# Kernel optimization log

Hardware: AMD Instinct MI355X
Metric: run time of the kernel (lower is better)

## Reference

```python
import jax, jax.numpy as jnp
import numpy as np

D = 1024   # model dim
H = 16     # heads
HD = D // H
L = 14     # layers
FF = 4096  # ffn hidden
T = 768    # sequence length


def layer_norm(x, g, b, eps):
    m = x.mean(-1, keepdims=True)
    v = ((x - m) ** 2).mean(-1, keepdims=True)
    return (x - m) / jnp.sqrt(v + eps) * g + b


def rel_pos_emb(t, d):
    # EspnetRelPositionalEncoding: concat(flip(pe_positive), pe_negative[1:]) -> (1, 2t-1, d)
    pos = jnp.arange(t, dtype=jnp.float32)
    div = jnp.exp(jnp.arange(0, d, 2, dtype=jnp.float32) * (-jnp.log(10000.0) / d))
    ang = pos[:, None] * div[None, :]                              # (t, d/2)
    pe_pos = jnp.stack([jnp.sin(ang), jnp.cos(ang)], -1).reshape(t, d)
    pe_neg = jnp.stack([jnp.sin(-ang), jnp.cos(-ang)], -1).reshape(t, d)
    return jnp.concatenate([pe_pos[::-1], pe_neg[1:]], 0)[None]    # (1, 2t-1, d)


def rel_shift(x):
    # x: (b, h, t, 2t-1) -> (b, h, t, t), Transformer-XL shift
    b, h, t, n = x.shape
    xp = jnp.concatenate([jnp.zeros((b, h, t, 1), x.dtype), x], -1)  # (b,h,t,n+1)
    xp = xp.reshape(b, h, n + 1, t)
    x = xp[:, :, 1:].reshape(b, h, t, n)
    return x[..., : n // 2 + 1]


def setup_inputs() -> dict:
    key = jax.random.key(0)
    ks = iter(jax.random.split(key, 40))
    s = 0.02
    nrm = lambda k, shape: jax.random.normal(k, shape, dtype=jnp.float32) * s
    return {
        "xs": jax.random.normal(next(ks), (1, T, D), dtype=jnp.float32),
        "embed_W": nrm(next(ks), (D, D)), "embed_b": jnp.zeros((D,), jnp.float32),
        "embed_ln_g": jnp.ones((D,), jnp.float32), "embed_ln_b": jnp.zeros((D,), jnp.float32),
        "Wq": nrm(next(ks), (L, D, D)), "bq": jnp.zeros((L, D), jnp.float32),
        "Wk": nrm(next(ks), (L, D, D)), "bk": jnp.zeros((L, D), jnp.float32),
        "Wv": nrm(next(ks), (L, D, D)), "bv": jnp.zeros((L, D), jnp.float32),
        "Wo": nrm(next(ks), (L, D, D)), "bo": jnp.zeros((L, D), jnp.float32),
        "Wp": nrm(next(ks), (L, D, D)),
        "pos_u": nrm(next(ks), (L, H, HD)), "pos_v": nrm(next(ks), (L, H, HD)),
        "ln1_g": jnp.ones((L, D), jnp.float32), "ln1_b": jnp.zeros((L, D), jnp.float32),
        "ln2_g": jnp.ones((L, D), jnp.float32), "ln2_b": jnp.zeros((L, D), jnp.float32),
        "ff_W1": nrm(next(ks), (L, D, FF)), "ff_b1": jnp.zeros((L, FF), jnp.float32),
        "ff_W2": nrm(next(ks), (L, FF, D)), "ff_b2": jnp.zeros((L, D), jnp.float32),
        "after_g": jnp.ones((D,), jnp.float32), "after_b": jnp.zeros((D,), jnp.float32),
    }


def reference(xs, embed_W, embed_b, embed_ln_g, embed_ln_b,
              Wq, bq, Wk, bk, Wv, bv, Wo, bo, Wp, pos_u, pos_v,
              ln1_g, ln1_b, ln2_g, ln2_b, ff_W1, ff_b1, ff_W2, ff_b2,
              after_g, after_b):
    b, t, _ = xs.shape
    # LegacyLinearNoSubsampling: Linear -> LayerNorm(eps=1e-5) -> (dropout) -> ReLU
    h = jnp.maximum(layer_norm(xs @ embed_W + embed_b, embed_ln_g, embed_ln_b, 1e-5), 0.0)
    x = h * jnp.sqrt(jnp.float32(D))          # pos-enc scale factor
    pos = rel_pos_emb(t, D)                    # (1, 2t-1, D)
    scale = jnp.float32(HD) ** -0.5
    for i in range(L):
        res = x
        xn = layer_norm(x, ln1_g[i], ln1_b[i], 1e-12)
        q = (xn @ Wq[i] + bq[i]).reshape(b, t, H, HD).transpose(0, 2, 1, 3)   # bhtd
        k = (xn @ Wk[i] + bk[i]).reshape(b, t, H, HD).transpose(0, 2, 1, 3)
        v = (xn @ Wv[i] + bv[i]).reshape(b, t, H, HD).transpose(0, 2, 1, 3)
        p = (pos @ Wp[i]).reshape(1, 2 * t - 1, H, HD).transpose(0, 2, 1, 3)  # bhnd
        ac = jnp.einsum('bhtd,bhsd->bhts', q + pos_u[i][None, :, None, :], k)
        bd = rel_shift(jnp.einsum('bhtd,bhnd->bhtn', q + pos_v[i][None, :, None, :], p))
        attn = jax.nn.softmax((ac + bd) * scale, axis=-1)
        o = jnp.einsum('bhts,bhsd->bhtd', attn, v).transpose(0, 2, 1, 3).reshape(b, t, D)
        x = res + (o @ Wo[i] + bo[i])
        res = x
        xn = layer_norm(x, ln2_g[i], ln2_b[i], 1e-12)
        x = res + (jnp.maximum(xn @ ff_W1[i] + ff_b1[i], 0.0) @ ff_W2[i] + ff_b2[i])
    return layer_norm(x, after_g, after_b, 1e-5)
```

## Files before the change

kernel.cpp:

```cpp
#include <hip/hip_runtime.h>
#include <hip/hip_bf16.h>
#include <math.h>

#define D_    1024
#define H_    16
#define HD_   64
#define L_    14
#define FF_   4096
#define T_    768
#define NPOS_ (2*T_-1)

using s16x8 = __attribute__((ext_vector_type(8))) short;
using f32x4 = __attribute__((ext_vector_type(4))) float;

__device__ inline short f2bf(float f) {
  __hip_bfloat16 h = __float2bfloat16(f);
  return *reinterpret_cast<short*>(&h);
}
__device__ inline float bf2f(unsigned short u) {
  union { unsigned u; float f; } v; v.u = ((unsigned)u) << 16; return v.f;
}

__device__ inline float waveRedSum(float v) {
#pragma unroll
  for (int o = 32; o > 0; o >>= 1) v += __shfl_down(v, o, 64);
  return v;
}
__device__ inline float blockRedSum(float v, float* sh) {
  int lane = threadIdx.x & 63, wid = threadIdx.x >> 6;
  v = waveRedSum(v);
  if (lane == 0) sh[wid] = v;
  __syncthreads();
  if (wid == 0) {
    float x = (lane < 4) ? sh[lane] : 0.f;
    x = waveRedSum(x);
    if (lane == 0) sh[0] = x;
  }
  __syncthreads();
  float r = sh[0];
  __syncthreads();
  return r;
}

__global__ __launch_bounds__(256) void ln_kernel(
    const float* __restrict__ x, const float* __restrict__ g,
    const float* __restrict__ b, void* __restrict__ y,
    float eps, int relu, float scale, int obf)
{
  __shared__ float sh[8];
  long row = blockIdx.x;
  const float* xr = x + row * D_;
  int tid = threadIdx.x;
  float4 v = *(const float4*)&xr[tid * 4];
  float s  = v.x + v.y + v.z + v.w;
  float sq = v.x * v.x + v.y * v.y + v.z * v.z + v.w * v.w;
  float mean = blockRedSum(s, sh) * (1.f / D_);
  float esq  = blockRedSum(sq, sh) * (1.f / D_);
  float var  = esq - mean * mean;
  if (var < 0.f) var = 0.f;
  float inv = rsqrtf(var + eps);
  float4 gv = *(const float4*)&g[tid * 4];
  float4 bv = *(const float4*)&b[tid * 4];
  float o0 = (v.x - mean) * inv * gv.x + bv.x;
  float o1 = (v.y - mean) * inv * gv.y + bv.y;
  float o2 = (v.z - mean) * inv * gv.z + bv.z;
  float o3 = (v.w - mean) * inv * gv.w + bv.w;
  if (relu) {
    o0 = fmaxf(o0, 0.f); o1 = fmaxf(o1, 0.f);
    o2 = fmaxf(o2, 0.f); o3 = fmaxf(o3, 0.f);
  }
  o0 *= scale; o1 *= scale; o2 *= scale; o3 *= scale;
  if (obf) {
    short4 sv;
    sv.x = f2bf(o0); sv.y = f2bf(o1); sv.z = f2bf(o2); sv.w = f2bf(o3);
    *(short4*)&((unsigned short*)y)[row * D_ + tid * 4] = sv;
  } else {
    float4 ov; ov.x = o0; ov.y = o1; ov.z = o2; ov.w = o3;
    *(float4*)&((float*)y)[row * D_ + tid * 4] = ov;
  }
}

__global__ __launch_bounds__(256) void transpose_kernel(
    const float* __restrict__ in, unsigned short* __restrict__ out, int K, int N)
{
  __shared__ unsigned short t[32][33];
  long z = blockIdx.z;
  in  += z * (long)K * N;
  out += z * (long)K * N;
  int n0 = blockIdx.x * 32, k0 = blockIdx.y * 32;
  int tid = threadIdx.x;
  int r = tid >> 3, c4 = (tid & 7) * 4;
  float4 v = *(const float4*)&in[(long)(k0 + r) * N + n0 + c4];
  t[r][c4 + 0] = (unsigned short)f2bf(v.x);
  t[r][c4 + 1] = (unsigned short)f2bf(v.y);
  t[r][c4 + 2] = (unsigned short)f2bf(v.z);
  t[r][c4 + 3] = (unsigned short)f2bf(v.w);
  __syncthreads();
  ushort4 s;
  s.x = t[c4 + 0][r]; s.y = t[c4 + 1][r]; s.z = t[c4 + 2][r]; s.w = t[c4 + 3][r];
  *(ushort4*)&out[(long)(n0 + r) * K + k0 + c4] = s;
}

__global__ __launch_bounds__(256) void transpose5_kernel(
    const float* __restrict__ W0, const float* __restrict__ W1,
    const float* __restrict__ W2, const float* __restrict__ W3,
    const float* __restrict__ W4,
    unsigned short* __restrict__ O0, unsigned short* __restrict__ O1,
    unsigned short* __restrict__ O2, unsigned short* __restrict__ O3,
    unsigned short* __restrict__ O4)
{
  __shared__ unsigned short t[32][33];
  int z = blockIdx.z;
  int g = z / L_, zi = z % L_;
  const float* in = (g == 0) ? W0 : (g == 1) ? W1 : (g == 2) ? W2 : (g == 3) ? W3 : W4;
  unsigned short* out = (g == 0) ? O0 : (g == 1) ? O1 : (g == 2) ? O2 : (g == 3) ? O3 : O4;
  in  += (long)zi * D_ * D_;
  out += (long)zi * D_ * D_;
  int n0 = blockIdx.x * 32, k0 = blockIdx.y * 32;
  int tid = threadIdx.x;
  int r = tid >> 3, c4 = (tid & 7) * 4;
  float4 v = *(const float4*)&in[(long)(k0 + r) * D_ + n0 + c4];
  t[r][c4 + 0] = (unsigned short)f2bf(v.x);
  t[r][c4 + 1] = (unsigned short)f2bf(v.y);
  t[r][c4 + 2] = (unsigned short)f2bf(v.z);
  t[r][c4 + 3] = (unsigned short)f2bf(v.w);
  __syncthreads();
  ushort4 s;
  s.x = t[c4 + 0][r]; s.y = t[c4 + 1][r]; s.z = t[c4 + 2][r]; s.w = t[c4 + 3][r];
  *(ushort4*)&out[(long)(n0 + r) * D_ + k0 + c4] = s;
}

template<int BM, int BN, bool CBF16>
__global__ __launch_bounds__(256) void gemm8_kernel(
    const unsigned short* __restrict__ A, int lda, long sAz,
    const unsigned short* __restrict__ B0, const unsigned short* __restrict__ B1,
    const unsigned short* __restrict__ B2, int ldb, long sBz,
    void* C0, void* C1, void* C2, int ldc, long sCz,
    const float* __restrict__ bias0, const float* __restrict__ bias1,
    const float* __restrict__ bias2,
    const float* __restrict__ resid, int ldres,
    int M, int N, int K, int zPerG, int relu, int nM)
{
  constexpr int FM = BM / 32, FN = BN / 32;
  constexpr int A_IT = BM / 32;
  constexpr int B_IT = BN / 32;

  __shared__ short As0[BM * 64];
  __shared__ short Bs0[BN * 64];
  __shared__ short As1[BM * 64];
  __shared__ short Bs1[BN * 64];

  int nb = gridDim.x, bid = blockIdx.x;
  int q = nb >> 3, r = nb & 7, xcd = bid & 7, idx = bid >> 3;
  int lbid = (xcd < r ? xcd * (q + 1) : r * (q + 1) + (xcd - r) * q) + idx;
  int mT = lbid % nM, nT = lbid / nM;
  int m0 = mT * BM, n0 = nT * BN;

  int z = blockIdx.z;
  int g = z / zPerG, zb = z - g * zPerG;
  A += (long)zb * sAz;
  const unsigned short* Bh = ((g == 0) ? B0 : ((g == 1) ? B1 : B2)) + zb * sBz;
  void* Cv = (g == 0) ? C0 : ((g == 1) ? C1 : C2);
  const float* bias = (g == 0) ? bias0 : ((g == 1) ? bias1 : bias2);
  float* Cf = (float*)Cv + zb * sCz;
  unsigned short* Ch = (unsigned short*)Cv + zb * sCz;

  int tid = threadIdx.x, lane = tid & 63, wid = tid >> 6;
  int wm0 = (wid >> 1) * (BM / 2), wn0 = (wid & 1) * (BN / 2);
  int lr = lane & 15, kl = (lane >> 4) * 8;

  f32x4 acc[FM][FN];
#pragma unroll
  for (int i = 0; i < FM; ++i)
#pragma unroll
    for (int j = 0; j < FN; ++j)
#pragma unroll
      for (int rr = 0; rr < 4; ++rr) acc[i][j][rr] = 0.f;

  s16x8 ar[A_IT], br[B_IT];

  auto loadT = [&](int k0) {
#pragma unroll
    for (int it = 0; it < A_IT; ++it) {
      int f = tid + it * 256;
      int row = f >> 3, c8 = f & 7;
      int gm = m0 + row;
      s16x8 v = {0, 0, 0, 0, 0, 0, 0, 0};
      if (gm < M) v = *(const s16x8*)(A + (long)gm * lda + k0 + c8 * 8);
      ar[it] = v;
    }
#pragma unroll
    for (int it = 0; it < B_IT; ++it) {
      int f = tid + it * 256;
      int row = f >> 3, c8 = f & 7;
      br[it] = *(const s16x8*)(Bh + (long)(n0 + row) * ldb + k0 + c8 * 8);
    }
  };
  auto writeT = [&](short* as, short* bs) {
#pragma unroll
    for (int it = 0; it < A_IT; ++it) {
      int f = tid + it * 256;
      int row = f >> 3, c8 = f & 7;
      *(s16x8*)&as[row * 64 + ((c8 ^ (row & 7)) << 3)] = ar[it];
    }
#pragma unroll
    for (int it = 0; it < B_IT; ++it) {
      int f = tid + it * 256;
      int row = f >> 3, c8 = f & 7;
      *(s16x8*)&bs[row * 64 + ((c8 ^ (row & 7)) << 3)] = br[it];
    }
  };
  auto compute = [&](const short* as, const short* bs) {
#pragma unroll
    for (int kk = 0; kk < 2; ++kk) {
      s16x8 a[FM], b[FN];
#pragma unroll
      for (int i = 0; i < FM; ++i) {
        int row = wm0 + i * 16 + lr;
        a[i] = *(const s16x8*)&as[row * 64 + ((kk * 32 + kl) ^ ((lr & 7) << 3))];
      }
#pragma unroll
      for (int j = 0; j < FN; ++j) {
        int row = wn0 + j * 16 + lr;
        b[j] = *(const s16x8*)&bs[row * 64 + ((kk * 32 + kl) ^ ((lr & 7) << 3))];
      }
#pragma unroll
      for (int i = 0; i < FM; ++i)
#pragma unroll
        for (int j = 0; j < FN; ++j)
          acc[i][j] = __builtin_amdgcn_mfma_f32_16x16x32_bf16(a[i], b[j], acc[i][j], 0, 0, 0);
    }
  };

  int nt = K / 64;
  loadT(0);
  writeT(As0, Bs0);
  __syncthreads();
  for (int t = 0; t < nt; t += 2) {
    loadT((t + 1) * 64);
    compute(As0, Bs0);
    writeT(As1, Bs1);
    __syncthreads();
    if (t + 2 < nt) loadT((t + 2) * 64);
    compute(As1, Bs1);
    if (t + 2 < nt) writeT(As0, Bs0);
    __syncthreads();
  }

#pragma unroll
  for (int i = 0; i < FM; ++i) {
#pragma unroll
    for (int j = 0; j < FN; ++j) {
      int n = n0 + wn0 + j * 16 + lr;
      float bv = bias ? bias[n] : 0.f;
#pragma unroll
      for (int rr = 0; rr < 4; ++rr) {
        int m = m0 + wm0 + i * 16 + (lane >> 4) * 4 + rr;
        if (m < M) {
          float v = acc[i][j][rr] + bv;
          if (resid) v += resid[(long)m * ldres + n];
          if (relu)  v = fmaxf(v, 0.f);
          if constexpr (CBF16) Ch[(long)m * ldc + n] = (unsigned short)f2bf(v);
          else                 Cf[(long)m * ldc + n] = v;
        }
      }
    }
  }
}

template<int BM, int BN, bool CBF16>
__global__ __launch_bounds__(256) void gemm5_kernel(
    const unsigned short* __restrict__ A, int lda, long sAz,
    const void* __restrict__ B0, const void* __restrict__ B1, const void* __restrict__ B2,
    int ldb, long sBz,
    void* C0, void* C1, void* C2, int ldc, long sCz,
    const float* __restrict__ bias0, const float* __restrict__ bias1,
    const float* __restrict__ bias2,
    const float* __restrict__ resid, int ldres,
    int M, int N, int K, int zPerG, int relu, int nM)
{
  constexpr int FM = BM / 32, FN = BN / 32;
  constexpr int A_IT = BM / 32;
  constexpr int NSH = (BN == 128) ? 7 : 6;

  __shared__ short As[BM * 64];
  __shared__ short Bs[BN * 64];

  int nb = gridDim.x, bid = blockIdx.x;
  int q = nb >> 3, r = nb & 7, xcd = bid & 7, idx = bid >> 3;
  int lbid = (xcd < r ? xcd * (q + 1) : r * (q + 1) + (xcd - r) * q) + idx;
  int mT = lbid % nM, nT = lbid / nM;
  int m0 = mT * BM, n0 = nT * BN;

  int z = blockIdx.z;
  int g = z / zPerG, zb = z - g * zPerG;
  A += (long)zb * sAz;
  const void* Bv = (g == 0) ? B0 : ((g == 1) ? B1 : B2);
  void* Cv       = (g == 0) ? C0 : ((g == 1) ? C1 : C2);
  const float* bias = (g == 0) ? bias0 : ((g == 1) ? bias1 : bias2);
  const float* Bf = (const float*)Bv + zb * sBz;
  float* Cf = (float*)Cv + zb * sCz;
  unsigned short* Ch = (unsigned short*)Cv + zb * sCz;

  int tid = threadIdx.x, lane = tid & 63, wid = tid >> 6;
  int wm0 = (wid >> 1) * (BM / 2), wn0 = (wid & 1) * (BN / 2);
  int lr = lane & 15, kl = (lane >> 4) * 8;

  f32x4 acc[FM][FN];
#pragma unroll
  for (int i = 0; i < FM; ++i)
#pragma unroll
    for (int j = 0; j < FN; ++j)
#pragma unroll
      for (int rr = 0; rr < 4; ++rr) acc[i][j][rr] = 0.f;

  for (int k0 = 0; k0 < K; k0 += 64) {
#pragma unroll
    for (int it = 0; it < A_IT; ++it) {
      int f = tid + it * 256;
      int row = f >> 3, c8 = f & 7;
      int gm = m0 + row;
      s16x8 v = {0, 0, 0, 0, 0, 0, 0, 0};
      if (gm < M) v = *(const s16x8*)(A + (long)gm * lda + k0 + c8 * 8);
      *(s16x8*)&As[row * 64 + ((c8 ^ (row & 7)) << 3)] = v;
    }
    constexpr int B_IT2 = BN / 16;
#pragma unroll
    for (int it = 0; it < B_IT2; ++it) {
      int p = tid + it * 256;
      int n = p & (BN - 1), kq = p >> NSH;
      int gn = n0 + n;
      const float* bp = Bf + (long)(k0 + kq * 4) * ldb + gn;
      short4 s;
      s.x = f2bf(bp[0]); s.y = f2bf(bp[ldb]);
      s.z = f2bf(bp[2 * (long)ldb]); s.w = f2bf(bp[3 * (long)ldb]);
      *(short4*)&Bs[n * 64 + ((kq << 2) ^ ((n & 7) << 3))] = s;
    }
    __syncthreads();
#pragma unroll
    for (int kk = 0; kk < 2; ++kk) {
      s16x8 a[FM], b[FN];
#pragma unroll
      for (int i = 0; i < FM; ++i) {
        int row = wm0 + i * 16 + lr;
        a[i] = *(const s16x8*)&As[row * 64 + ((kk * 32 + kl) ^ ((lr & 7) << 3))];
      }
#pragma unroll
      for (int j = 0; j < FN; ++j) {
        int row = wn0 + j * 16 + lr;
        b[j] = *(const s16x8*)&Bs[row * 64 + ((kk * 32 + kl) ^ ((lr & 7) << 3))];
      }
#pragma unroll
      for (int i = 0; i < FM; ++i)
#pragma unroll
        for (int j = 0; j < FN; ++j)
          acc[i][j] = __builtin_amdgcn_mfma_f32_16x16x32_bf16(a[i], b[j], acc[i][j], 0, 0, 0);
    }
    __syncthreads();
  }
#pragma unroll
  for (int i = 0; i < FM; ++i) {
#pragma unroll
    for (int j = 0; j < FN; ++j) {
      int n = n0 + wn0 + j * 16 + lr;
      float bv = bias ? bias[n] : 0.f;
#pragma unroll
      for (int rr = 0; rr < 4; ++rr) {
        int m = m0 + wm0 + i * 16 + (lane >> 4) * 4 + rr;
        if (m < M) {
          float v = acc[i][j][rr] + bv;
          if (resid) v += resid[(long)m * ldres + n];
          if (relu)  v = fmaxf(v, 0.f);
          if constexpr (CBF16) Ch[(long)m * ldc + n] = (unsigned short)f2bf(v);
          else                 Cf[(long)m * ldc + n] = v;
        }
      }
    }
  }
}

__global__ __launch_bounds__(256) void f2bf_kernel(
    const float* __restrict__ x, unsigned short* __restrict__ y, int n4)
{
  int i = blockIdx.x * 256 + threadIdx.x;
  if (i >= n4) return;
  float4 v = *(const float4*)&x[i * 4];
  short4 s; s.x = f2bf(v.x); s.y = f2bf(v.y); s.z = f2bf(v.z); s.w = f2bf(v.w);
  *(short4*)&y[i * 4] = s;
}

__global__ __launch_bounds__(256) void pos_kernel(unsigned short* __restrict__ pos)
{
  int idx = blockIdx.x * 256 + threadIdx.x;
  if (idx >= NPOS_ * (D_ / 2)) return;
  int n = idx / (D_ / 2), i = idx % (D_ / 2);
  float r = (float)(T_ - 1 - n);
  float div = __expf((float)(2 * i) * (-logf(10000.f) / (float)D_));
  float ang = r * div;
  pos[(long)n * D_ + 2 * i]     = (unsigned short)f2bf(sinf(ang));
  pos[(long)n * D_ + 2 * i + 1] = (unsigned short)f2bf(cosf(ang));
}

__global__ __launch_bounds__(256) void flash_attn_kernel(
    const unsigned short* __restrict__ Q, const unsigned short* __restrict__ K,
    const unsigned short* __restrict__ V, const unsigned short* __restrict__ P,
    const float* __restrict__ posu, const float* __restrict__ posv,
    unsigned short* __restrict__ O)
{
  __shared__ short Ks[64 * 64];
  __shared__ short Vs[64 * 64];
  __shared__ short Ps[96 * 64];
  __shared__ float Grgn[32 * 99];
  __shared__ float mxls[2][32], smls[2][32];

  short* qu = (short*)Grgn;
  short* qv = qu + 32 * 64;
  float* G  = Grgn;
  short* Pf = (short*)Grgn;

  int h = blockIdx.y;
  int t0 = blockIdx.x * 32;
  int tid = threadIdx.x, lane = tid & 63, w = tid >> 6;
  int wr = w >> 1, wc = w & 1;
  int lr = lane & 15, lg = lane >> 4;
  int kl = lg * 8;
  const float* pu = posu + h * HD_;
  const float* pv = posv + h * HD_;

  {
    int row = tid >> 3, c8 = tid & 7;
    s16x8 q8 = *(const s16x8*)(Q + (long)(t0 + row) * D_ + h * HD_ + c8 * 8);
    const unsigned short* qp = (const unsigned short*)&q8;
    s16x8 su, sv;
#pragma unroll
    for (int j = 0; j < 8; ++j) {
      float qf = bf2f(qp[j]);
      su[j] = f2bf(qf + pu[c8 * 8 + j]);
      sv[j] = f2bf(qf + pv[c8 * 8 + j]);
    }
    int sw = row * 64 + ((c8 ^ (row & 7)) << 3);
    *(s16x8*)&qu[sw] = su;
    *(s16x8*)&qv[sw] = sv;
  }
  __syncthreads();
  s16x8 aqu[2], aqv[2];
#pragma unroll
  for (int kk = 0; kk < 2; ++kk) {
    int row = wr * 16 + lr;
    int col = (kk * 32 + kl) ^ ((lr & 7) << 3);
    aqu[kk] = *(const s16x8*)&qu[row * 64 + col];
    aqv[kk] = *(const s16x8*)&qv[row * 64 + col];
  }

  float m_[4], l_[4];
  f32x4 acc_o[2];
#pragma unroll
  for (int rr = 0; rr < 4; ++rr) { m_[rr] = -1e30f; l_[rr] = 0.f; }
#pragma unroll
  for (int j = 0; j < 2; ++j)
#pragma unroll
    for (int rr = 0; rr < 4; ++rr) acc_o[j][rr] = 0.f;

  for (int s0 = 0; s0 < T_; s0 += 64) {
    int base = s0 - t0 + T_ - 32;
    __syncthreads();
#pragma unroll
    for (int it = 0; it < 2; ++it) {
      int f = tid + it * 256;
      int row = f >> 3, c8 = f & 7;
      s16x8 v = *(const s16x8*)(K + (long)(s0 + row) * D_ + h * HD_ + c8 * 8);
      *(s16x8*)&Ks[row * 64 + ((c8 ^ (row & 7)) << 3)] = v;
    }
#pragma unroll
    for (int it = 0; it < 4; ++it) {
      int d = tid & 63, sq = tid >> 6;
      int s = it * 16 + sq * 4;
      const unsigned short* vp = V + (long)(s0 + s) * D_ + h * HD_ + d;
      short4 sv4;
      sv4.x = (short)vp[0];
      sv4.y = (short)vp[D_];
      sv4.z = (short)vp[2 * D_];
      sv4.w = (short)vp[3 * D_];
      *(short4*)&Vs[d * 64 + (s ^ ((d & 7) << 3))] = sv4;
    }
#pragma unroll
    for (int it = 0; it < 3; ++it) {
      int f = tid + it * 256;
      int row = f >> 3, c8 = f & 7;
      int gp = base + row; if (gp > NPOS_ - 1) gp = NPOS_ - 1;
      s16x8 v = *(const s16x8*)(P + (long)gp * D_ + h * HD_ + c8 * 8);
      *(s16x8*)&Ps[row * 64 + ((c8 ^ (row & 7)) << 3)] = v;
    }
    __syncthreads();
    f32x4 a_ac[2], a_g[3];
#pragma unroll
    for (int j = 0; j < 2; ++j)
#pragma unroll
      for (int rr = 0; rr < 4; ++rr) a_ac[j][rr] = 0.f;
#pragma unroll
    for (int j = 0; j < 3; ++j)
#pragma unroll
      for (int rr = 0; rr < 4; ++rr) a_g[j][rr] = 0.f;
#pragma unroll
    for (int j = 0; j < 2; ++j)
#pragma unroll
      for (int kk = 0; kk < 2; ++kk) {
        int row = wc * 32 + j * 16 + lr;
        s16x8 b = *(const s16x8*)&Ks[row * 64 + ((kk * 32 + kl) ^ ((lr & 7) << 3))];
        a_ac[j] = __builtin_amdgcn_mfma_f32_16x16x32_bf16(aqu[kk], b, a_ac[j], 0, 0, 0);
      }
#pragma unroll
    for (int j = 0; j < 3; ++j)
#pragma unroll
      for (int kk = 0; kk < 2; ++kk) {
        int row = wc * 48 + j * 16 + lr;
        s16x8 b = *(const s16x8*)&Ps[row * 64 + ((kk * 32 + kl) ^ ((lr & 7) << 3))];
        a_g[j] = __builtin_amdgcn_mfma_f32_16x16x32_bf16(aqv[kk], b, a_g[j], 0, 0, 0);
      }
#pragma unroll
    for (int j = 0; j < 3; ++j)
#pragma unroll
      for (int rr = 0; rr < 4; ++rr) {
        int row = wr * 16 + lg * 4 + rr;
        int col = wc * 48 + j * 16 + lr;
        G[row * 99 + col] = a_g[j][rr];
      }
    __syncthreads();
    float sreg[2][4], pm[4];
#pragma unroll
    for (int rr = 0; rr < 4; ++rr) {
      int row = wr * 16 + lg * 4 + rr;
#pragma unroll
      for (int j = 0; j < 2; ++j) {
        int c = wc * 32 + j * 16 + lr;
        int gc = c - row + 31;
        sreg[j][rr] = (a_ac[j][rr] + G[row * 99 + gc]) * 0.125f;
      }
      pm[rr] = fmaxf(sreg[0][rr], sreg[1][rr]);
    }
#pragma unroll
    for (int o = 1; o < 16; o <<= 1)
#pragma unroll
      for (int rr = 0; rr < 4; ++rr) pm[rr] = fmaxf(pm[rr], __shfl_xor(pm[rr], o, 64));
    if (lr == 0) {
#pragma unroll
      for (int rr = 0; rr < 4; ++rr) mxls[wc][wr * 16 + lg * 4 + rr] = pm[rr];
    }
    __syncthreads();
    float ps[4];
#pragma unroll
    for (int rr = 0; rr < 4; ++rr) {
      int row = wr * 16 + lg * 4 + rr;
      float mnew = fmaxf(m_[rr], fmaxf(mxls[0][row], mxls[1][row]));
      float sc = __expf(m_[rr] - mnew);
      m_[rr] = mnew;
      l_[rr] *= sc;
      acc_o[0][rr] *= sc;
      acc_o[1][rr] *= sc;
      float p0 = __expf(sreg[0][rr] - mnew);
      float p1 = __expf(sreg[1][rr] - mnew);
      ps[rr] = p0 + p1;
      int c0 = wc * 32 + lr, c1 = wc * 32 + 16 + lr;
      ((unsigned short*)Pf)[row * 64 + (c0 ^ ((row & 7) << 3))] = (unsigned short)f2bf(p0);
      ((unsigned short*)Pf)[row * 64 + (c1 ^ ((row & 7) << 3))] = (unsigned short)f2bf(p1);
    }
#pragma unroll
    for (int o = 1; o < 16; o <<= 1)
#pragma unroll
      for (int rr = 0; rr < 4; ++rr) ps[rr] += __shfl_xor(ps[rr], o, 64);
    if (lr == 0) {
#pragma unroll
      for (int rr = 0; rr < 4; ++rr) smls[wc][wr * 16 + lg * 4 + rr] = ps[rr];
    }
    __syncthreads();
#pragma unroll
    for (int rr = 0; rr < 4; ++rr) {
      int row = wr * 16 + lg * 4 + rr;
      l_[rr] += smls[0][row] + smls[1][row];
    }
    s16x8 ap[2];
#pragma unroll
    for (int kk = 0; kk < 2; ++kk) {
      int row = wr * 16 + lr;
      ap[kk] = *(const s16x8*)&((unsigned short*)Pf)[row * 64 + ((kk * 32 + kl) ^ ((lr & 7) << 3))];
    }
#pragma unroll
    for (int j = 0; j < 2; ++j)
#pragma unroll
      for (int kk = 0; kk < 2; ++kk) {
        int row = wc * 32 + j * 16 + lr;
        s16x8 b = *(const s16x8*)&Vs[row * 64 + ((kk * 32 + kl) ^ ((lr & 7) << 3))];
        acc_o[j] = __builtin_amdgcn_mfma_f32_16x16x32_bf16(ap[kk], b, acc_o[j], 0, 0, 0);
      }
  }
#pragma unroll
  for (int j = 0; j < 2; ++j)
#pragma unroll
    for (int rr = 0; rr < 4; ++rr) {
      int row = t0 + wr * 16 + lg * 4 + rr;
      int col = h * HD_ + wc * 32 + j * 16 + lr;
      O[(long)row * D_ + col] = (unsigned short)f2bf(acc_o[j][rr] / l_[rr]);
    }
}

extern "C" void kernel_launch(void* const* d_in, const int* in_sizes, int n_in,
                              void* d_out, int out_size, void* d_ws, size_t ws_size,
                              hipStream_t stream) {
  const float* xs       = (const float*)d_in[0];
  const float* embed_W  = (const float*)d_in[1];
  const float* embed_b  = (const float*)d_in[2];
  const float* embed_g  = (const float*)d_in[3];
  const float* embed_bt = (const float*)d_in[4];
  const float* Wq = (const float*)d_in[5];
  const float* bq = (const float*)d_in[6];
  const float* Wk = (const float*)d_in[7];
  const float* bk = (const float*)d_in[8];
  const float* Wv = (const float*)d_in[9];
  const float* bv = (const float*)d_in[10];
  const float* Wo = (const float*)d_in[11];
  const float* bo = (const float*)d_in[12];
  const float* Wp = (const float*)d_in[13];
  const float* pos_u = (const float*)d_in[14];
  const float* pos_v = (const float*)d_in[15];
  const float* ln1_g = (const float*)d_in[16];
  const float* ln1_b = (const float*)d_in[17];
  const float* ln2_g = (const float*)d_in[18];
  const float* ln2_b = (const float*)d_in[19];
  const float* ff_W1 = (const float*)d_in[20];
  const float* ff_b1 = (const float*)d_in[21];
  const float* ff_W2 = (const float*)d_in[22];
  const float* ff_b2 = (const float*)d_in[23];
  const float* after_g = (const float*)d_in[24];
  const float* after_b = (const float*)d_in[25];
  float* out = (float*)d_out;

  char* w = (char*)d_ws;
  auto carve = [&](size_t bytes) { char* p = w; w += (bytes + 255) & ~(size_t)255; return p; };
  float* bufX  = (float*)carve((size_t)T_ * D_ * 4);
  float* bufT  = (float*)carve((size_t)T_ * D_ * 4);
  unsigned short* xsb  = (unsigned short*)carve((size_t)T_ * D_ * 2);
  unsigned short* XNb  = (unsigned short*)carve((size_t)T_ * D_ * 2);
  unsigned short* Qb   = (unsigned short*)carve((size_t)T_ * D_ * 2);
  unsigned short* Kb   = (unsigned short*)carve((size_t)T_ * D_ * 2);
  unsigned short* Vb   = (unsigned short*)carve((size_t)T_ * D_ * 2);
  unsigned short* Ob   = (unsigned short*)carve((size_t)T_ * D_ * 2);
  unsigned short* Hb   = (unsigned short*)carve((size_t)T_ * FF_ * 2);
  unsigned short* posT = (unsigned short*)carve((size_t)(NPOS_ + 16) * D_ * 2);
  unsigned short* Pall = (unsigned short*)carve((size_t)L_ * NPOS_ * D_ * 2);
  size_t szDD = (size_t)D_ * D_;
  unsigned short* embedWt = (unsigned short*)carve(szDD * 2);
  unsigned short* WqT = (unsigned short*)carve((size_t)L_ * szDD * 2);
  unsigned short* WkT = (unsigned short*)carve((size_t)L_ * szDD * 2);
  unsigned short* WvT = (unsigned short*)carve((size_t)L_ * szDD * 2);
  unsigned short* WoT = (unsigned short*)carve((size_t)L_ * szDD * 2);
  unsigned short* WpT = (unsigned short*)carve((size_t)L_ * szDD * 2);
  unsigned short* W1T = (unsigned short*)carve((size_t)L_ * D_ * FF_ * 2);
  unsigned short* W2T = (unsigned short*)carve((size_t)L_ * D_ * FF_ * 2);
  bool fast = ((size_t)(w - (char*)d_ws) <= ws_size);

  {
    int n = NPOS_ * (D_ / 2);
    pos_kernel<<<(n + 255) / 256, 256, 0, stream>>>(posT);
  }
  f2bf_kernel<<<(T_ * D_ / 4 + 255) / 256, 256, 0, stream>>>(xs, xsb, T_ * D_ / 4);

  if (fast) {
    transpose_kernel<<<dim3(32, 32, 1),  256, 0, stream>>>(embed_W, embedWt, D_, D_);
    transpose5_kernel<<<dim3(32, 32, 5 * L_), 256, 0, stream>>>(
        Wq, Wk, Wv, Wo, Wp, WqT, WkT, WvT, WoT, WpT);
    transpose_kernel<<<dim3(128, 32, L_), 256, 0, stream>>>(ff_W1, W1T, D_, FF_);
    transpose_kernel<<<dim3(32, 128, L_), 256, 0, stream>>>(ff_W2, W2T, FF_, D_);

    gemm8_kernel<32, 128, false><<<dim3(192, 1, 1), 256, 0, stream>>>(
        xsb, D_, 0, embedWt, nullptr, nullptr, D_, 0,
        bufT, nullptr, nullptr, D_, 0, embed_b, nullptr, nullptr,
        nullptr, 0, T_, D_, D_, 1, 0, 24);
    ln_kernel<<<T_, 256, 0, stream>>>(bufT, embed_g, embed_bt, bufX, 1e-5f, 1, 32.0f, 0);

    gemm8_kernel<128, 64, true><<<dim3(192, 1, 14), 256, 0, stream>>>(
        posT, D_, 0, WpT, nullptr, nullptr, D_, (long)szDD,
        Pall, nullptr, nullptr, D_, (long)NPOS_ * D_, nullptr, nullptr, nullptr,
        nullptr, 0, NPOS_, D_, D_, 14, 0, 12);

    for (int i = 0; i < L_; ++i) {
      ln_kernel<<<T_, 256, 0, stream>>>(bufX, ln1_g + (long)i * D_, ln1_b + (long)i * D_,
                                        XNb, 1e-12f, 0, 1.0f, 1);
      gemm8_kernel<32, 128, true><<<dim3(192, 1, 3), 256, 0, stream>>>(
          XNb, D_, 0, WqT + i * szDD, WkT + i * szDD, WvT + i * szDD, D_, 0,
          Qb, Kb, Vb, D_, 0,
          bq + (long)i * D_, bk + (long)i * D_, bv + (long)i * D_,
          nullptr, 0, T_, D_, D_, 1, 0, 24);
      flash_attn_kernel<<<dim3(T_ / 32, H_), 256, 0, stream>>>(
          Qb, Kb, Vb, Pall + (long)i * NPOS_ * D_,
          pos_u + (long)i * D_, pos_v + (long)i * D_, Ob);
      gemm8_kernel<32, 64, false><<<dim3(384, 1, 1), 256, 0, stream>>>(
          Ob, D_, 0, WoT + i * szDD, nullptr, nullptr, D_, 0,
          bufX, nullptr, nullptr, D_, 0, bo + (long)i * D_, nullptr, nullptr,
          bufX, D_, T_, D_, D_, 1, 0, 24);
      ln_kernel<<<T_, 256, 0, stream>>>(bufX, ln2_g + (long)i * D_, ln2_b + (long)i * D_,
                                        XNb, 1e-12f, 0, 1.0f, 1);
      gemm8_kernel<32, 128, true><<<dim3(768, 1, 1), 256, 0, stream>>>(
          XNb, D_, 0, W1T + (size_t)i * D_ * FF_, nullptr, nullptr, D_, 0,
          Hb, nullptr, nullptr, FF_, 0, ff_b1 + (long)i * FF_, nullptr, nullptr,
          nullptr, 0, T_, FF_, D_, 1, 1, 24);
      gemm8_kernel<32, 64, false><<<dim3(384, 1, 1), 256, 0, stream>>>(
          Hb, FF_, 0, W2T + (size_t)i * D_ * FF_, nullptr, nullptr, FF_, 0,
          bufX, nullptr, nullptr, D_, 0, ff_b2 + (long)i * D_, nullptr, nullptr,
          bufX, D_, T_, FF_, FF_, 1, 0, 24);
    }
  } else {
    gemm5_kernel<32, 128, false><<<dim3(192, 1, 1), 256, 0, stream>>>(
        xsb, D_, 0, embed_W, nullptr, nullptr, D_, 0,
        bufT, nullptr, nullptr, D_, 0, embed_b, nullptr, nullptr,
        nullptr, 0, T_, D_, D_, 1, 0, 24);
    ln_kernel<<<T_, 256, 0, stream>>>(bufT, embed_g, embed_bt, bufX, 1e-5f, 1, 32.0f, 0);

    gemm5_kernel<128, 64, true><<<dim3(192, 1, 14), 256, 0, stream>>>(
        posT, D_, 0, Wp, nullptr, nullptr, D_, (long)szDD,
        Pall, nullptr, nullptr, D_, (long)NPOS_ * D_, nullptr, nullptr, nullptr,
        nullptr, 0, NPOS_, D_, D_, 14, 0, 12);

    for (int i = 0; i < L_; ++i) {
      ln_kernel<<<T_, 256, 0, stream>>>(bufX, ln1_g + (long)i * D_, ln1_b + (long)i * D_,
                                        XNb, 1e-12f, 0, 1.0f, 1);
      gemm5_kernel<32, 128, true><<<dim3(192, 1, 3), 256, 0, stream>>>(
          XNb, D_, 0, Wq + i * szDD, Wk + i * szDD, Wv + i * szDD, D_, 0,
          Qb, Kb, Vb, D_, 0,
          bq + (long)i * D_, bk + (long)i * D_, bv + (long)i * D_,
          nullptr, 0, T_, D_, D_, 1, 0, 24);
      flash_attn_kernel<<<dim3(T_ / 32, H_), 256, 0, stream>>>(
          Qb, Kb, Vb, Pall + (long)i * NPOS_ * D_,
          pos_u + (long)i * D_, pos_v + (long)i * D_, Ob);
      gemm5_kernel<32, 64, false><<<dim3(384, 1, 1), 256, 0, stream>>>(
          Ob, D_, 0, Wo + i * szDD, nullptr, nullptr, D_, 0,
          bufX, nullptr, nullptr, D_, 0, bo + (long)i * D_, nullptr, nullptr,
          bufX, D_, T_, D_, D_, 1, 0, 24);
      ln_kernel<<<T_, 256, 0, stream>>>(bufX, ln2_g + (long)i * D_, ln2_b + (long)i * D_,
                                        XNb, 1e-12f, 0, 1.0f, 1);
      gemm5_kernel<32, 128, true><<<dim3(768, 1, 1), 256, 0, stream>>>(
          XNb, D_, 0, ff_W1 + (size_t)i * D_ * FF_, nullptr, nullptr, FF_, 0,
          Hb, nullptr, nullptr, FF_, 0, ff_b1 + (long)i * FF_, nullptr, nullptr,
          nullptr, 0, T_, FF_, D_, 1, 1, 24);
      gemm5_kernel<32, 64, false><<<dim3(384, 1, 1), 256, 0, stream>>>(
          Hb, FF_, 0, ff_W2 + (size_t)i * D_ * FF_, nullptr, nullptr, D_, 0,
          bufX, nullptr, nullptr, D_, 0, ff_b2 + (long)i * D_, nullptr, nullptr,
          bufX, D_, T_, FF_, FF_, 1, 0, 24);
    }
  }

  ln_kernel<<<T_, 256, 0, stream>>>(bufX, after_g, after_b, out, 1e-5f, 0, 1.0f, 0);
}
```

Before: 2.442 ms.

## Give each attention wave full rows to drop cross-wave softmax syncs

New measurement: 3.239 ms. +32.6%, slower.

```diff
diff --git a/kernel.cpp b/kernel.cpp
--- a/kernel.cpp
+++ b/kernel.cpp
@@ -401,7 +401,7 @@
   pos[(long)n * D_ + 2 * i + 1] = (unsigned short)f2bf(cosf(ang));
 }
 
-__global__ __launch_bounds__(256) void flash_attn_kernel(
+__global__ __launch_bounds__(128) void flash_attn_kernel(
     const unsigned short* __restrict__ Q, const unsigned short* __restrict__ K,
     const unsigned short* __restrict__ V, const unsigned short* __restrict__ P,
     const float* __restrict__ posu, const float* __restrict__ posv,
@@ -410,25 +410,22 @@
   __shared__ short Ks[64 * 64];
   __shared__ short Vs[64 * 64];
   __shared__ short Ps[96 * 64];
-  __shared__ float Grgn[32 * 99];
-  __shared__ float mxls[2][32], smls[2][32];
-
-  short* qu = (short*)Grgn;
+  __shared__ unsigned short Gb[32 * 128];
+  __shared__ short Pf[32 * 64];
+  short* qu = (short*)Gb;
   short* qv = qu + 32 * 64;
-  float* G  = Grgn;
-  short* Pf = (short*)Grgn;
 
   int h = blockIdx.y;
   int t0 = blockIdx.x * 32;
   int tid = threadIdx.x, lane = tid & 63, w = tid >> 6;
-  int wr = w >> 1, wc = w & 1;
-  int lr = lane & 15, lg = lane >> 4;
-  int kl = lg * 8;
+  int lr = lane & 15, lg = lane >> 4, kl = lg * 8;
   const float* pu = posu + h * HD_;
   const float* pv = posv + h * HD_;
 
-  {
-    int row = tid >> 3, c8 = tid & 7;
+#pragma unroll
+  for (int it = 0; it < 2; ++it) {
+    int f = tid + it * 128;
+    int row = f >> 3, c8 = f & 7;
     s16x8 q8 = *(const s16x8*)(Q + (long)(t0 + row) * D_ + h * HD_ + c8 * 8);
     const unsigned short* qp = (const unsigned short*)&q8;
     s16x8 su, sv;
@@ -446,18 +443,18 @@
   s16x8 aqu[2], aqv[2];
 #pragma unroll
   for (int kk = 0; kk < 2; ++kk) {
-    int row = wr * 16 + lr;
+    int row = w * 16 + lr;
     int col = (kk * 32 + kl) ^ ((lr & 7) << 3);
     aqu[kk] = *(const s16x8*)&qu[row * 64 + col];
     aqv[kk] = *(const s16x8*)&qv[row * 64 + col];
   }
 
   float m_[4], l_[4];
-  f32x4 acc_o[2];
+  f32x4 acc_o[4];
 #pragma unroll
   for (int rr = 0; rr < 4; ++rr) { m_[rr] = -1e30f; l_[rr] = 0.f; }
 #pragma unroll
-  for (int j = 0; j < 2; ++j)
+  for (int j = 0; j < 4; ++j)
 #pragma unroll
     for (int rr = 0; rr < 4; ++rr) acc_o[j][rr] = 0.f;
 
@@ -465,16 +462,16 @@
     int base = s0 - t0 + T_ - 32;
     __syncthreads();
 #pragma unroll
-    for (int it = 0; it < 2; ++it) {
-      int f = tid + it * 256;
+    for (int it = 0; it < 4; ++it) {
+      int f = tid + it * 128;
       int row = f >> 3, c8 = f & 7;
       s16x8 v = *(const s16x8*)(K + (long)(s0 + row) * D_ + h * HD_ + c8 * 8);
       *(s16x8*)&Ks[row * 64 + ((c8 ^ (row & 7)) << 3)] = v;
     }
 #pragma unroll
-    for (int it = 0; it < 4; ++it) {
+    for (int it = 0; it < 8; ++it) {
       int d = tid & 63, sq = tid >> 6;
-      int s = it * 16 + sq * 4;
+      int s = it * 8 + sq * 4;
       const unsigned short* vp = V + (long)(s0 + s) * D_ + h * HD_ + d;
       short4 sv4;
       sv4.x = (short)vp[0];
@@ -484,121 +481,114 @@
       *(short4*)&Vs[d * 64 + (s ^ ((d & 7) << 3))] = sv4;
     }
 #pragma unroll
-    for (int it = 0; it < 3; ++it) {
-      int f = tid + it * 256;
+    for (int it = 0; it < 6; ++it) {
+      int f = tid + it * 128;
       int row = f >> 3, c8 = f & 7;
       int gp = base + row; if (gp > NPOS_ - 1) gp = NPOS_ - 1;
       s16x8 v = *(const s16x8*)(P + (long)gp * D_ + h * HD_ + c8 * 8);
       *(s16x8*)&Ps[row * 64 + ((c8 ^ (row & 7)) << 3)] = v;
     }
     __syncthreads();
-    f32x4 a_ac[2], a_g[3];
-#pragma unroll
-    for (int j = 0; j < 2; ++j)
+    f32x4 a_ac[4];
+#pragma unroll
+    for (int j = 0; j < 4; ++j)
 #pragma unroll
       for (int rr = 0; rr < 4; ++rr) a_ac[j][rr] = 0.f;
 #pragma unroll
-    for (int j = 0; j < 3; ++j)
-#pragma unroll
-      for (int rr = 0; rr < 4; ++rr) a_g[j][rr] = 0.f;
-#pragma unroll
-    for (int j = 0; j < 2; ++j)
+    for (int j = 0; j < 4; ++j)
 #pragma unroll
       for (int kk = 0; kk < 2; ++kk) {
-        int row = wc * 32 + j * 16 + lr;
+        int row = j * 16 + lr;
         s16x8 b = *(const s16x8*)&Ks[row * 64 + ((kk * 32 + kl) ^ ((lr & 7) << 3))];
         a_ac[j] = __builtin_amdgcn_mfma_f32_16x16x32_bf16(aqu[kk], b, a_ac[j], 0, 0, 0);
       }
-#pragma unroll
-    for (int j = 0; j < 3; ++j)
+    f32x4 a_g[6];
+#pragma unroll
+    for (int j = 0; j < 6; ++j)
+#pragma unroll
+      for (int rr = 0; rr < 4; ++rr) a_g[j][rr] = 0.f;
+#pragma unroll
+    for (int j = 0; j < 6; ++j)
 #pragma unroll
       for (int kk = 0; kk < 2; ++kk) {
-        int row = wc * 48 + j * 16 + lr;
+        int row = j * 16 + lr;
         s16x8 b = *(const s16x8*)&Ps[row * 64 + ((kk * 32 + kl) ^ ((lr & 7) << 3))];
         a_g[j] = __builtin_amdgcn_mfma_f32_16x16x32_bf16(aqv[kk], b, a_g[j], 0, 0, 0);
       }
 #pragma unroll
-    for (int j = 0; j < 3; ++j)
+    for (int j = 0; j < 6; ++j)
 #pragma unroll
       for (int rr = 0; rr < 4; ++rr) {
-        int row = wr * 16 + lg * 4 + rr;
-        int col = wc * 48 + j * 16 + lr;
-        G[row * 99 + col] = a_g[j][rr];
-      }
-    __syncthreads();
-    float sreg[2][4], pm[4];
+        int row = w * 16 + lg * 4 + rr;
+        int col = j * 16 + lr;
+        Gb[row * 128 + (col ^ ((row & 7) << 3))] = (unsigned short)f2bf(a_g[j][rr]);
+      }
+    float sreg[4][4], pm[4];
 #pragma unroll
     for (int rr = 0; rr < 4; ++rr) {
-      int row = wr * 16 + lg * 4 + rr;
-#pragma unroll
-      for (int j = 0; j < 2; ++j) {
-        int c = wc * 32 + j * 16 + lr;
-        int gc = c - row + 31;
-        sreg[j][rr] = (a_ac[j][rr] + G[row * 99 + gc]) * 0.125f;
-      }
-      pm[rr] = fmaxf(sreg[0][rr], sreg[1][rr]);
+      int row = w * 16 + lg * 4 + rr;
+      int lrow = lg * 4 + rr + w * 16;
+      float mx = -1e30f;
+#pragma unroll
+      for (int j = 0; j < 4; ++j) {
+        int c = j * 16 + lr;
+        int gc = c - (lrow) + 31;
+        float bd = bf2f(Gb[row * 128 + (gc ^ ((row & 7) << 3))]);
+        sreg[j][rr] = (a_ac[j][rr] + bd) * 0.125f;
+        mx = fmaxf(mx, sreg[j][rr]);
+      }
+      pm[rr] = mx;
     }
 #pragma unroll
     for (int o = 1; o < 16; o <<= 1)
 #pragma unroll
       for (int rr = 0; rr < 4; ++rr) pm[rr] = fmaxf(pm[rr], __shfl_xor(pm[rr], o, 64));
-    if (lr == 0) {
-#pragma unroll
-      for (int rr = 0; rr < 4; ++rr) mxls[wc][wr * 16 + lg * 4 + rr] = pm[rr];
-    }
-    __syncthreads();
     float ps[4];
 #pragma unroll
     for (int rr = 0; rr < 4; ++rr) {
-      int row = wr * 16 + lg * 4 + rr;
-      float mnew = fmaxf(m_[rr], fmaxf(mxls[0][row], mxls[1][row]));
+      int row = w * 16 + lg * 4 + rr;
+      float mnew = fmaxf(m_[rr], pm[rr]);
       float sc = __expf(m_[rr] - mnew);
       m_[rr] = mnew;
       l_[rr] *= sc;
-      acc_o[0][rr] *= sc;
-      acc_o[1][rr] *= sc;
-      float p0 = __expf(sreg[0][rr] - mnew);
-      float p1 = __expf(sreg[1][rr] - mnew);
-      ps[rr] = p0 + p1;
-      int c0 = wc * 32 + lr, c1 = wc * 32 + 16 + lr;
-      ((unsigned short*)Pf)[row * 64 + (c0 ^ ((row & 7) << 3))] = (unsigned short)f2bf(p0);
-      ((unsigned short*)Pf)[row * 64 + (c1 ^ ((row & 7) << 3))] = (unsigned short)f2bf(p1);
+#pragma unroll
+      for (int jf = 0; jf < 4; ++jf) acc_o[jf][rr] *= sc;
+      ps[rr] = 0.f;
+#pragma unroll
+      for (int j = 0; j < 4; ++j) {
+        float p = __expf(sreg[j][rr] - mnew);
+        ps[rr] += p;
+        int c = j * 16 + lr;
+        ((unsigned short*)Pf)[row * 64 + (c ^ ((row & 7) << 3))] = (unsigned short)f2bf(p);
+      }
     }
 #pragma unroll
     for (int o = 1; o < 16; o <<= 1)
 #pragma unroll
       for (int rr = 0; rr < 4; ++rr) ps[rr] += __shfl_xor(ps[rr], o, 64);
-    if (lr == 0) {
-#pragma unroll
-      for (int rr = 0; rr < 4; ++rr) smls[wc][wr * 16 + lg * 4 + rr] = ps[rr];
-    }
-    __syncthreads();
-#pragma unroll
-    for (int rr = 0; rr < 4; ++rr) {
-      int row = wr * 16 + lg * 4 + rr;
-      l_[rr] += smls[0][row] + smls[1][row];
-    }
+#pragma unroll
+    for (int rr = 0; rr < 4; ++rr) l_[rr] += ps[rr];
     s16x8 ap[2];
 #pragma unroll
     for (int kk = 0; kk < 2; ++kk) {
-      int row = wr * 16 + lr;
+      int row = w * 16 + lr;
       ap[kk] = *(const s16x8*)&((unsigned short*)Pf)[row * 64 + ((kk * 32 + kl) ^ ((lr & 7) << 3))];
     }
 #pragma unroll
-    for (int j = 0; j < 2; ++j)
+    for (int j = 0; j < 4; ++j)
 #pragma unroll
       for (int kk = 0; kk < 2; ++kk) {
-        int row = wc * 32 + j * 16 + lr;
+        int row = j * 16 + lr;
         s16x8 b = *(const s16x8*)&Vs[row * 64 + ((kk * 32 + kl) ^ ((lr & 7) << 3))];
         acc_o[j] = __builtin_amdgcn_mfma_f32_16x16x32_bf16(ap[kk], b, acc_o[j], 0, 0, 0);
       }
   }
 #pragma unroll
-  for (int j = 0; j < 2; ++j)
+  for (int j = 0; j < 4; ++j)
 #pragma unroll
     for (int rr = 0; rr < 4; ++rr) {
-      int row = t0 + wr * 16 + lg * 4 + rr;
-      int col = h * HD_ + wc * 32 + j * 16 + lr;
+      int row = t0 + w * 16 + lg * 4 + rr;
+      int col = h * HD_ + j * 16 + lr;
       O[(long)row * D_ + col] = (unsigned short)f2bf(acc_o[j][rr] / l_[rr]);
     }
 }
@@ -690,7 +680,7 @@
           Qb, Kb, Vb, D_, 0,
           bq + (long)i * D_, bk + (long)i * D_, bv + (long)i * D_,
           nullptr, 0, T_, D_, D_, 1, 0, 24);
-      flash_attn_kernel<<<dim3(T_ / 32, H_), 256, 0, stream>>>(
+      flash_attn_kernel<<<dim3(T_ / 32, H_), 128, 0, stream>>>(
           Qb, Kb, Vb, Pall + (long)i * NPOS_ * D_,
           pos_u + (long)i * D_, pos_v + (long)i * D_, Ob);
       gemm8_kernel<32, 64, false><<<dim3(384, 1, 1), 256, 0, stream>>>(
@@ -728,7 +718,7 @@
           Qb, Kb, Vb, D_, 0,
           bq + (long)i * D_, bk + (long)i * D_, bv + (long)i * D_,
           nullptr, 0, T_, D_, D_, 1, 0, 24);
-      flash_attn_kernel<<<dim3(T_ / 32, H_), 256, 0, stream>>>(
+      flash_attn_kernel<<<dim3(T_ / 32, H_), 128, 0, stream>>>(
           Qb, Kb, Vb, Pall + (long)i * NPOS_ * D_,
           pos_u + (long)i * D_, pos_v + (long)i * D_, Ob);
       gemm5_kernel<32, 64, false><<<dim3(384, 1, 1), 256, 0, stream>>>(
```
